# Optimization experiments

Hardware: AMD Instinct MI355X
Metric: run time of the kernel (lower is better)

The kernel has to match this reference:

```python
import jax, jax.numpy as jnp
import numpy as np
from jax import lax

# Geometry constants (stand-in for beijing* globals)
A = 96           # beijingAngleNum
P = 4            # beijingPlanes
DET0, DET1 = 256, 8   # beijingSubDetectorSize [u, v]
NZ, NY, NX = 32, 256, 256  # beijingVolumeSize (nz = P * DET1)
T = 256          # ray integration steps
LAMB = 0.01


def _bilinear(vol, ix, iy):
    # vol: [nz, ny, nx]; ix, iy: [...] index-space coords. Zero outside.
    nz, ny, nx = vol.shape
    x0 = jnp.floor(ix); y0 = jnp.floor(iy)
    fx = (ix - x0).astype(vol.dtype); fy = (iy - y0).astype(vol.dtype)
    x0i = x0.astype(jnp.int32); y0i = y0.astype(jnp.int32)

    def g(yi, xi):
        valid = ((xi >= 0) & (xi < nx) & (yi >= 0) & (yi < ny)).astype(vol.dtype)
        v = vol[:, jnp.clip(yi, 0, ny - 1), jnp.clip(xi, 0, nx - 1)]  # [nz, ...]
        return v * valid

    return (g(y0i, x0i) * (1 - fy) * (1 - fx)
            + g(y0i, x0i + 1) * (1 - fy) * fx
            + g(y0i + 1, x0i) * fy * (1 - fx)
            + g(y0i + 1, x0i + 1) * fy * fx)


def forward_project(vol):
    # vol: [NZ, NY, NX] -> sinogram [A, NZ, DET0], parallel-beam over 180 deg
    angles = jnp.arange(A, dtype=jnp.float32) * (np.pi / A)
    u = jnp.arange(DET0, dtype=jnp.float32) - (DET0 - 1) / 2.0  # detector coord
    t = jnp.arange(T, dtype=jnp.float32) - (T - 1) / 2.0        # along-ray coord

    def per_angle(_, th):
        c, s = jnp.cos(th), jnp.sin(th)
        x = -u[:, None] * s + t[None, :] * c   # [DET0, T]
        y = u[:, None] * c + t[None, :] * s
        samp = _bilinear(vol, x + (NX - 1) / 2.0, y + (NY - 1) / 2.0)  # [NZ,DET0,T]
        return None, samp.sum(-1)  # line integral, [NZ, DET0]

    _, S = lax.scan(per_angle, None, angles)
    return S  # [A, NZ, DET0]


def back_project(S):
    # S: [A, NZ, DET0] -> volume [NZ, NY, NX] (adjoint-style backprojection)
    angles = jnp.arange(A, dtype=jnp.float32) * (np.pi / A)
    yy = jnp.arange(NY, dtype=jnp.float32) - (NY - 1) / 2.0
    xx = jnp.arange(NX, dtype=jnp.float32) - (NX - 1) / 2.0
    Y, X = jnp.meshgrid(yy, xx, indexing='ij')  # [NY, NX]

    def per_angle(acc, inp):
        th, Sa = inp  # Sa: [NZ, DET0]
        c, s = jnp.cos(th), jnp.sin(th)
        ub = -X * s + Y * c + (DET0 - 1) / 2.0  # detector bin coord [NY,NX]
        u0 = jnp.floor(ub)
        fu = (ub - u0).astype(Sa.dtype)
        u0i = u0.astype(jnp.int32)

        def g(ui):
            valid = ((ui >= 0) & (ui < DET0)).astype(Sa.dtype)
            return Sa[:, jnp.clip(ui, 0, DET0 - 1)] * valid  # [NZ,NY,NX]

        val = g(u0i) * (1 - fu) + g(u0i + 1) * fu
        return acc + val, None

    vol0 = jnp.zeros((NZ, NY, NX), dtype=S.dtype)
    vol, _ = lax.scan(per_angle, vol0, (angles, S))
    return vol


def setup_inputs() -> dict:
    key = jax.random.key(0)
    k1, k2 = jax.random.split(key)
    x = jax.random.normal(k1, (1, 1, NZ, NY, NX), dtype=jnp.float32)
    p = jax.random.normal(k2, (1, 1, A * P, DET1, DET0), dtype=jnp.float32)
    return {"x": x, "p": p}


def reference(x, p):
    vol = x[0, 0]                              # [NZ, NY, NX]
    S = forward_project(vol)                   # [A, NZ, DET0] native
    # ForwardProjection wrapper: (A,P,V,U) -> permute -> flat external layout
    ext = S.reshape(A, P, DET1, DET0).transpose(0, 2, 1, 3).reshape(1, 1, A * P, DET1, DET0)
    residual = ext - p
    # BackProjection wrapper: undo external layout back to native
    res_native = residual.reshape(A, DET1, P, DET0).transpose(0, 2, 1, 3).reshape(A, NZ, DET0)
    volb = back_project(res_native)            # [NZ, NY, NX]
    return (-LAMB * volb)[None, None]          # [1,1,NZ,NY,NX]
```

## Files before the change

### kernel.cpp

```cpp
#include <hip/hip_runtime.h>
#include <hip/hip_fp16.h>

#define A     96
#define DET0  256
#define NZ    32
#define NY    256
#define NX    256
#define T     256
#define LAMB  0.01f

#define TRIG_OFF  0
#define REST_OFF  256
#define VOLB_OFF  786688
#define PART_OFF  1835264
#define RES_ELEMS 786432

__device__ __forceinline__ void accp_mix(float& a0, float& a1, unsigned v, float w) {
    asm("v_fma_mix_f32 %0, %2, %3, %0 op_sel:[0,0,0] op_sel_hi:[1,0,0]\n\t"
        "v_fma_mix_f32 %1, %2, %3, %1 op_sel:[1,0,0] op_sel_hi:[1,0,0]"
        : "+v"(a0), "+v"(a1)
        : "v"(v), "v"(w));
}
__device__ __forceinline__ void acc8h(float* acc, uint4 q, float w) {
    accp_mix(acc[0], acc[1], q.x, w);
    accp_mix(acc[2], acc[3], q.y, w);
    accp_mix(acc[4], acc[5], q.z, w);
    accp_mix(acc[6], acc[7], q.w, w);
}

__global__ __launch_bounds__(256) void k_transpose(const float* __restrict__ src,
                                                   unsigned short* __restrict__ vol_h,
                                                   float* __restrict__ trig,
                                                   const float* __restrict__ p,
                                                   float* __restrict__ res_t) {
    __shared__ float lds[64 * 33];
    const int y   = blockIdx.y;
    const int x0  = blockIdx.x * 64;
    const int tid = threadIdx.x;

    if (blockIdx.x == 0 && y == 0 && tid < A) {
        float th = (float)tid * (float)(3.14159265358979323846 / (double)A);
        trig[2 * tid]     = cosf(th);
        trig[2 * tid + 1] = sinf(th);
    }

    const int xr = tid & 63;
    const int zr = tid >> 6;
    #pragma unroll
    for (int pz = 0; pz < 8; ++pz) {
        int z = pz * 4 + zr;
        lds[xr * 33 + z] = src[(z * NY + y) * NX + x0 + xr];
    }
    __syncthreads();
    const int zw = tid & 31;
    const int xw = tid >> 5;
    #pragma unroll
    for (int px = 0; px < 8; ++px) {
        int xi = px * 8 + xw;
        vol_h[(y * NX + x0 + xi) * NZ + zw] =
            __half_as_ushort(__float2half(lds[xi * 33 + zw]));
    }

    if (y < A) {
        const int a  = y;
        const int u0 = blockIdx.x * 64;
        __syncthreads();
        const int col = tid & 63;
        const int r0  = tid >> 6;
        #pragma unroll
        for (int i = 0; i < 8; ++i) {
            int r = i * 4 + r0;
            lds[r * 65 + col] = p[a * 8192 + r * 256 + u0 + col];
        }
        __syncthreads();
        const int ul = tid >> 2;
        const int zb = (tid & 3) * 8;
        float o[8];
        #pragma unroll
        for (int k = 0; k < 8; ++k) {
            int z = zb + k;
            int r = ((z & 7) << 2) + (z >> 3);
            o[k] = -lds[r * 65 + ul];
        }
        float4* d = (float4*)(res_t + (a * DET0 + u0 + ul) * NZ + zb);
        d[0] = make_float4(o[0], o[1], o[2], o[3]);
        d[1] = make_float4(o[4], o[5], o[6], o[7]);
    }
}

__device__ __forceinline__ void rng(float g, float b, float L, float H,
                                    float& lo, float& hi) {
    if (fabsf(g) > 1e-5f) {
        float r0 = (L - b) / g, r1 = (H - b) / g;
        lo = fminf(r0, r1); hi = fmaxf(r0, r1);
    } else {
        bool in = (b >= L && b <= H);
        lo = in ? -1e9f : 1e9f;
        hi = in ? 1e9f : -1e9f;
    }
}
__device__ __forceinline__ int clampi(float v) {
    return (int)fminf(fmaxf(v, -2.f), 258.f);
}

__device__ __forceinline__ void sample_edge(const char* base, float ix, float iy,
                                            float* acc) {
    float xf = floorf(ix), yf = floorf(iy);
    float fx = ix - xf, fy = iy - yf;
    int x0 = (int)xf, y0 = (int)yf;
    float wx0 = 1.f - fx, wx1 = fx, wy0 = 1.f - fy, wy1 = fy;
    if ((unsigned)x0 >= NX)       wx0 = 0.f;
    if ((unsigned)(x0 + 1) >= NX) wx1 = 0.f;
    if ((unsigned)y0 >= NY)       wy0 = 0.f;
    if ((unsigned)(y0 + 1) >= NY) wy1 = 0.f;
    if ((wx0 == 0.f && wx1 == 0.f) || (wy0 == 0.f && wy1 == 0.f)) return;
    int cx0 = min(max(x0, 0), NX - 1);
    int cx1 = min(max(x0 + 1, 0), NX - 1);
    int cy0 = min(max(y0, 0), NY - 1);
    int cy1 = min(max(y0 + 1, 0), NY - 1);
    uint4 q00 = *(const uint4*)(base + ((size_t)((cy0 << 8) + cx0) << 6));
    uint4 q01 = *(const uint4*)(base + ((size_t)((cy0 << 8) + cx1) << 6));
    uint4 q10 = *(const uint4*)(base + ((size_t)((cy1 << 8) + cx0) << 6));
    uint4 q11 = *(const uint4*)(base + ((size_t)((cy1 << 8) + cx1) << 6));
    acc8h(acc, q00, wy0 * wx0);
    acc8h(acc, q01, wy0 * wx1);
    acc8h(acc, q10, wy1 * wx0);
    acc8h(acc, q11, wy1 * wx1);
}

__global__ __launch_bounds__(256) void k_forward(const unsigned short* __restrict__ vol_h,
                                                 const float* __restrict__ trig,
                                                 float* __restrict__ part) {
    const int tid = threadIdx.x;
    const int a   = blockIdx.z;
    const int u   = blockIdx.x * 64 + (tid >> 2);
    const int zq  = tid & 3;
    const int cid = blockIdx.y;
    const int C   = gridDim.y;

    const float c = trig[2 * a];
    const float s = trig[2 * a + 1];
    const float uu = (float)u - 127.5f;
    const float bx = fmaf(-uu, s, 127.5f);
    const float by = fmaf(uu, c, 127.5f);

    float lo1, hi1, lo2, hi2;
    rng(c, bx, -1.f, 256.f, lo1, hi1);
    rng(s, by, -1.f, 256.f, lo2, hi2);
    float fl = fmaxf(lo1, lo2), fh = fminf(hi1, hi2);
    int F0 = max(0,     clampi(ceilf(fl + 127.5f)));
    int F1 = min(T - 1, clampi(floorf(fh + 127.5f)));
    int len = F1 - F0 + 1; if (len < 0) len = 0;
    int b0 = F0 + (len * cid) / C;
    int b1 = F0 + (len * (cid + 1)) / C - 1;
    rng(c, bx, 1.f, 253.5f, lo1, hi1);
    rng(s, by, 1.f, 253.5f, lo2, hi2);
    float il = fmaxf(lo1, lo2), ih = fminf(hi1, hi2);
    int tI0 = max(clampi(ceilf(il + 127.5f)) + 1, b0);
    int tI1 = min(clampi(floorf(ih + 127.5f)) - 1, b1);
    if (tI0 > tI1) { tI0 = b1 + 1; tI1 = b1; }

    const char* base = (const char*)vol_h + zq * 16;
    float acc[8];
    #pragma unroll
    for (int k = 0; k < 8; ++k) acc[k] = 0.f;

    for (int t = b0; t < tI0; ++t) {
        float ttf = (float)t - 127.5f;
        sample_edge(base, fmaf(ttf, c, bx), fmaf(ttf, s, by), acc);
    }
    for (int t = tI0; t <= tI1; ++t) {
        float ttf = (float)t - 127.5f;
        float ix = fmaf(ttf, c, bx);
        float iy = fmaf(ttf, s, by);
        float xf = floorf(ix), yf = floorf(iy);
        float fx = ix - xf, fy = iy - yf;
        int row = ((int)yf << 8) + (int)xf;
        const char* p0 = base + ((size_t)row << 6);
        uint4 q00 = *(const uint4*)(p0);
        uint4 q01 = *(const uint4*)(p0 + 64);
        uint4 q10 = *(const uint4*)(p0 + 16384);
        uint4 q11 = *(const uint4*)(p0 + 16384 + 64);
        float wx0 = 1.f - fx, wy0 = 1.f - fy;
        acc8h(acc, q00, wy0 * wx0);
        acc8h(acc, q01, wy0 * fx);
        acc8h(acc, q10, fy * wx0);
        acc8h(acc, q11, fy * fx);
    }
    for (int t = tI1 + 1; t <= b1; ++t) {
        float ttf = (float)t - 127.5f;
        sample_edge(base, fmaf(ttf, c, bx), fmaf(ttf, s, by), acc);
    }

    float4* dst = (float4*)(part + (size_t)cid * RES_ELEMS +
                            ((a * DET0 + u) * NZ + zq * 8));
    dst[0] = make_float4(acc[0], acc[1], acc[2], acc[3]);
    dst[1] = make_float4(acc[4], acc[5], acc[6], acc[7]);
}

__global__ __launch_bounds__(256) void k_combine(const float* __restrict__ part,
                                                 float* __restrict__ res_t,
                                                 int C) {
    const int j4 = blockIdx.x * 256 + threadIdx.x;
    float4 v = ((const float4*)res_t)[j4];
    for (int c = 0; c < C; ++c) {
        float4 w = ((const float4*)(part + (size_t)c * RES_ELEMS))[j4];
        v.x += w.x; v.y += w.y; v.z += w.z; v.w += w.w;
    }
    ((float4*)res_t)[j4] = v;
}

__global__ __launch_bounds__(256) void k_backward(const float* __restrict__ res_t,
                                                  const float* __restrict__ trig,
                                                  float* __restrict__ out) {
    __shared__ float2 wbw[A * 32];
    __shared__ int    wbo[A * 32];
    __shared__ float  ob[32 * 33];
    const int tid = threadIdx.x;
    const int y  = blockIdx.y;
    const int xb = blockIdx.x * 32;

    for (int e = tid; e < A * 32; e += 256) {
        int a  = e >> 5;
        int xs = e & 31;
        float cc = trig[2 * a];
        float ss = trig[2 * a + 1];
        float xx = (float)(xb + xs) - 127.5f;
        float yy = (float)y - 127.5f;
        float ub = fmaf(-xx, ss, fmaf(yy, cc, 127.5f));
        float uf = floorf(ub);
        float fu = ub - uf;
        int i0 = (int)uf;
        float w0 = ((unsigned)i0 < DET0) ? (1.f - fu) : 0.f;
        float w1 = ((unsigned)(i0 + 1) < DET0) ? fu : 0.f;
        int c1 = min(max(i0 + 1, 0), DET0);
        wbw[e] = make_float2(w0, w1);
        wbo[e] = ((a * DET0 + c1) * NZ - NZ) << 2;
    }
    __syncthreads();

    const int xs = tid >> 3;
    const int zq = tid & 7;
    const char* rbase = (const char*)res_t + zq * 16;
    float4 acc = make_float4(0.f, 0.f, 0.f, 0.f);
    #pragma unroll 4
    for (int a = 0; a < A; ++a) {
        float2 w  = wbw[a * 32 + xs];
        int   off = wbo[a * 32 + xs];
        float4 v0 = *(const float4*)(rbase + off);
        float4 v1 = *(const float4*)(rbase + off + 128);
        acc.x = fmaf(w.x, v0.x, fmaf(w.y, v1.x, acc.x));
        acc.y = fmaf(w.x, v0.y, fmaf(w.y, v1.y, acc.y));
        acc.z = fmaf(w.x, v0.z, fmaf(w.y, v1.z, acc.z));
        acc.w = fmaf(w.x, v0.w, fmaf(w.y, v1.w, acc.w));
    }

    ob[(zq * 4 + 0) * 33 + xs] = acc.x;
    ob[(zq * 4 + 1) * 33 + xs] = acc.y;
    ob[(zq * 4 + 2) * 33 + xs] = acc.z;
    ob[(zq * 4 + 3) * 33 + xs] = acc.w;
    __syncthreads();

    const int z  = tid >> 3;
    const int x4 = (tid & 7) * 4;
    float4 o = make_float4(ob[z * 33 + x4],     ob[z * 33 + x4 + 1],
                           ob[z * 33 + x4 + 2], ob[z * 33 + x4 + 3]);
    float4* dst = (float4*)(out + (size_t)z * (NY * NX) + y * NX + xb + x4);
    *dst = make_float4(-LAMB * o.x, -LAMB * o.y, -LAMB * o.z, -LAMB * o.w);
}

extern "C" void kernel_launch(void* const* d_in, const int* in_sizes, int n_in,
                              void* d_out, int out_size, void* d_ws, size_t ws_size,
                              hipStream_t stream) {
    const float* x = (const float*)d_in[0];
    const float* p = (const float*)d_in[1];
    float* out = (float*)d_out;
    float* ws  = (float*)d_ws;

    float*          trig  = ws + TRIG_OFF;
    float*          res_t = ws + REST_OFF;
    unsigned short* vol_h = (unsigned short*)(ws + VOLB_OFF);
    float*          part  = ws + PART_OFF;

    size_t avail = ws_size / 4;
    int C = 8;
    while (C > 1 && (size_t)PART_OFF + (size_t)C * RES_ELEMS > avail) C >>= 1;

    k_transpose<<<dim3(NX / 64, NY), 256, 0, stream>>>(x, vol_h, trig, p, res_t);
    k_forward  <<<dim3(4, C, A), 256, 0, stream>>>(vol_h, trig, part);
    k_combine  <<<dim3(RES_ELEMS / 4 / 256), 256, 0, stream>>>(part, res_t, C);
    k_backward <<<dim3(NX / 32, NY), 256, 0, stream>>>(res_t, trig, out);
}
```

Measured before the change: 196.2 us.

## Stage per-angle detector windows in LDS with double buffering for backprojection

The backprojection kernel now handles two output rows per block. For each angle it computes the detector-bin window the 32x2 pixel tile touches and cooperatively loads that window of residual rows into XOR-swizzled shared memory, double-buffered so the next angle's global load overlaps the current angle's compute. This replaces the per-thread scattered global gathers and the precomputed weight tables with shared-memory reads and inline weight computation. The trade-offs are one barrier per angle, half as many blocks, and a fixed window size of 36 rows that has to cover every angle's footprint.

```diff
diff --git a/kernel.cpp b/kernel.cpp
--- a/kernel.cpp
+++ b/kernel.cpp
@@ -210,63 +210,135 @@
     ((float4*)res_t)[j4] = v;
 }
 
+#define BWIN 36
+#define BROW 144
 __global__ __launch_bounds__(256) void k_backward(const float* __restrict__ res_t,
                                                   const float* __restrict__ trig,
                                                   float* __restrict__ out) {
-    __shared__ float2 wbw[A * 32];
-    __shared__ int    wbo[A * 32];
-    __shared__ float  ob[32 * 33];
+    __shared__ float smem[2 * BWIN * (BROW / 4)];
     const int tid = threadIdx.x;
-    const int y  = blockIdx.y;
-    const int xb = blockIdx.x * 32;
-
-    for (int e = tid; e < A * 32; e += 256) {
-        int a  = e >> 5;
-        int xs = e & 31;
-        float cc = trig[2 * a];
-        float ss = trig[2 * a + 1];
-        float xx = (float)(xb + xs) - 127.5f;
-        float yy = (float)y - 127.5f;
-        float ub = fmaf(-xx, ss, fmaf(yy, cc, 127.5f));
-        float uf = floorf(ub);
-        float fu = ub - uf;
-        int i0 = (int)uf;
-        float w0 = ((unsigned)i0 < DET0) ? (1.f - fu) : 0.f;
-        float w1 = ((unsigned)(i0 + 1) < DET0) ? fu : 0.f;
-        int c1 = min(max(i0 + 1, 0), DET0);
-        wbw[e] = make_float2(w0, w1);
-        wbo[e] = ((a * DET0 + c1) * NZ - NZ) << 2;
-    }
+    const int xb  = blockIdx.x * 32;
+    const int y0  = blockIdx.y * 2;
+    const int xs  = tid >> 3;
+    const int zq  = tid & 7;
+    const float xt  = (float)(xb + xs) - 127.5f;
+    const float yt0 = (float)y0 - 127.5f;
+    const float yt1 = yt0 + 1.0f;
+    const float xlo = (float)xb - 127.5f;
+    const float xhi = (float)(xb + 31) - 127.5f;
+
+    float4 acc0 = make_float4(0.f, 0.f, 0.f, 0.f);
+    float4 acc1 = make_float4(0.f, 0.f, 0.f, 0.f);
+
+    #define WINDOW(aa, U0v, nchv) {                                        \
+        float cc_ = trig[2 * (aa)], ss_ = trig[2 * (aa) + 1];              \
+        float k0_ = fmaf(yt0, cc_, 127.5f);                                \
+        float k1_ = fmaf(yt1, cc_, 127.5f);                                \
+        float u00 = fmaf(-xlo, ss_, k0_), u01 = fmaf(-xhi, ss_, k0_);      \
+        float u10 = fmaf(-xlo, ss_, k1_), u11 = fmaf(-xhi, ss_, k1_);      \
+        float mn = fminf(fminf(u00, u01), fminf(u10, u11));                \
+        float mx = fmaxf(fmaxf(u00, u01), fmaxf(u10, u11));                \
+        U0v = (int)floorf(mn);                                             \
+        int rows_ = (int)floorf(mx) + 2 - U0v;   \
+        nchv = rows_ * 8;                         \
+    }
+    #define STAGE_LOAD(aa, U0v, nchv, r0, r1) {                            \
+        if (tid < (nchv)) {                                                \
+            int rr = tid >> 3, sl = tid & 7;                               \
+            int row = min(max((U0v) + rr, 0), DET0 - 1);                   \
+            r0 = *(const float4*)(res_t + (((aa) * DET0 + row) << 5) + sl * 4); \
+        }                                                                  \
+        if (tid + 256 < (nchv)) {                                          \
+            int cch = tid + 256;                                           \
+            int rr = cch >> 3, sl = cch & 7;                               \
+            int row = min(max((U0v) + rr, 0), DET0 - 1);                   \
+            r1 = *(const float4*)(res_t + (((aa) * DET0 + row) << 5) + sl * 4); \
+        }                                                                  \
+    }
+    #define STAGE_WRITE(bufv, nchv, r0, r1) {                              \
+        char* bb = (char*)(smem + (bufv) * (BWIN * BROW / 4));             \
+        if (tid < (nchv)) {                                                \
+            int rr = tid >> 3, sl = tid & 7;                               \
+            *(float4*)(bb + rr * BROW + ((sl ^ (rr & 7)) << 4)) = r0;      \
+        }                                                                  \
+        if (tid + 256 < (nchv)) {                                          \
+            int cch = tid + 256;                                           \
+            int rr = cch >> 3, sl = cch & 7;                               \
+            *(float4*)(bb + rr * BROW + ((sl ^ (rr & 7)) << 4)) = r1;      \
+        }                                                                  \
+    }
+
+    int U0c, nchc, U0n, nchn;
+    float4 s0, s1;
+    WINDOW(0, U0c, nchc);
+    STAGE_LOAD(0, U0c, nchc, s0, s1);
+    STAGE_WRITE(0, nchc, s0, s1);
     __syncthreads();
 
-    const int xs = tid >> 3;
-    const int zq = tid & 7;
-    const char* rbase = (const char*)res_t + zq * 16;
-    float4 acc = make_float4(0.f, 0.f, 0.f, 0.f);
-    #pragma unroll 4
     for (int a = 0; a < A; ++a) {
-        float2 w  = wbw[a * 32 + xs];
-        int   off = wbo[a * 32 + xs];
-        float4 v0 = *(const float4*)(rbase + off);
-        float4 v1 = *(const float4*)(rbase + off + 128);
-        acc.x = fmaf(w.x, v0.x, fmaf(w.y, v1.x, acc.x));
-        acc.y = fmaf(w.x, v0.y, fmaf(w.y, v1.y, acc.y));
-        acc.z = fmaf(w.x, v0.z, fmaf(w.y, v1.z, acc.z));
-        acc.w = fmaf(w.x, v0.w, fmaf(w.y, v1.w, acc.w));
-    }
-
-    ob[(zq * 4 + 0) * 33 + xs] = acc.x;
-    ob[(zq * 4 + 1) * 33 + xs] = acc.y;
-    ob[(zq * 4 + 2) * 33 + xs] = acc.z;
-    ob[(zq * 4 + 3) * 33 + xs] = acc.w;
-    __syncthreads();
-
-    const int z  = tid >> 3;
-    const int x4 = (tid & 7) * 4;
-    float4 o = make_float4(ob[z * 33 + x4],     ob[z * 33 + x4 + 1],
-                           ob[z * 33 + x4 + 2], ob[z * 33 + x4 + 3]);
-    float4* dst = (float4*)(out + (size_t)z * (NY * NX) + y * NX + xb + x4);
-    *dst = make_float4(-LAMB * o.x, -LAMB * o.y, -LAMB * o.z, -LAMB * o.w);
+        const int cur = a & 1;
+        if (a + 1 < A) {
+            WINDOW(a + 1, U0n, nchn);
+            STAGE_LOAD(a + 1, U0n, nchn, s0, s1);
+        }
+        const float cc = trig[2 * a];
+        const float ss = trig[2 * a + 1];
+        const char* bb = (const char*)(smem + cur * (BWIN * BROW / 4));
+        {
+            float ub = fmaf(-xt, ss, fmaf(yt0, cc, 127.5f));
+            float uf = floorf(ub);
+            float fu = ub - uf;
+            int i0 = (int)uf;
+            float w0 = ((unsigned)i0 < DET0) ? (1.f - fu) : 0.f;
+            float w1 = ((unsigned)(i0 + 1) < DET0) ? fu : 0.f;
+            int idx = i0 - U0c;
+            int id1 = idx + 1;
+            float4 v0 = *(const float4*)(bb + idx * BROW + ((zq ^ (idx & 7)) << 4));
+            float4 v1 = *(const float4*)(bb + id1 * BROW + ((zq ^ (id1 & 7)) << 4));
+            acc0.x = fmaf(w0, v0.x, fmaf(w1, v1.x, acc0.x));
+            acc0.y = fmaf(w0, v0.y, fmaf(w1, v1.y, acc0.y));
+            acc0.z = fmaf(w0, v0.z, fmaf(w1, v1.z, acc0.z));
+            acc0.w = fmaf(w0, v0.w, fmaf(w1, v1.w, acc0.w));
+        }
+        {
+            float ub = fmaf(-xt, ss, fmaf(yt1, cc, 127.5f));
+            float uf = floorf(ub);
+            float fu = ub - uf;
+            int i0 = (int)uf;
+            float w0 = ((unsigned)i0 < DET0) ? (1.f - fu) : 0.f;
+            float w1 = ((unsigned)(i0 + 1) < DET0) ? fu : 0.f;
+            int idx = i0 - U0c;
+            int id1 = idx + 1;
+            float4 v0 = *(const float4*)(bb + idx * BROW + ((zq ^ (idx & 7)) << 4));
+            float4 v1 = *(const float4*)(bb + id1 * BROW + ((zq ^ (id1 & 7)) << 4));
+            acc1.x = fmaf(w0, v0.x, fmaf(w1, v1.x, acc1.x));
+            acc1.y = fmaf(w0, v0.y, fmaf(w1, v1.y, acc1.y));
+            acc1.z = fmaf(w0, v0.z, fmaf(w1, v1.z, acc1.z));
+            acc1.w = fmaf(w0, v0.w, fmaf(w1, v1.w, acc1.w));
+        }
+        if (a + 1 < A) {
+            STAGE_WRITE(cur ^ 1, nchn, s0, s1);
+            U0c = U0n;
+        }
+        __syncthreads();
+    }
+
+    #pragma unroll 1
+    for (int yt = 0; yt < 2; ++yt) {
+        float4 acc = yt ? acc1 : acc0;
+        smem[(zq * 4 + 0) * 33 + xs] = acc.x;
+        smem[(zq * 4 + 1) * 33 + xs] = acc.y;
+        smem[(zq * 4 + 2) * 33 + xs] = acc.z;
+        smem[(zq * 4 + 3) * 33 + xs] = acc.w;
+        __syncthreads();
+        int z  = tid >> 3;
+        int x4 = (tid & 7) * 4;
+        float4 o = make_float4(smem[z * 33 + x4],     smem[z * 33 + x4 + 1],
+                               smem[z * 33 + x4 + 2], smem[z * 33 + x4 + 3]);
+        float4* dst = (float4*)(out + (size_t)z * (NY * NX) + (y0 + yt) * NX + xb + x4);
+        *dst = make_float4(-LAMB * o.x, -LAMB * o.y, -LAMB * o.z, -LAMB * o.w);
+        __syncthreads();
+    }
 }
 
 extern "C" void kernel_launch(void* const* d_in, const int* in_sizes, int n_in,
@@ -289,5 +361,5 @@
     k_transpose<<<dim3(NX / 64, NY), 256, 0, stream>>>(x, vol_h, trig, p, res_t);
     k_forward  <<<dim3(4, C, A), 256, 0, stream>>>(vol_h, trig, part);
     k_combine  <<<dim3(RES_ELEMS / 4 / 256), 256, 0, stream>>>(part, res_t, C);
-    k_backward <<<dim3(NX / 32, NY), 256, 0, stream>>>(res_t, trig, out);
-}
+    k_backward <<<dim3(NX / 32, NY / 2), 256, 0, stream>>>(res_t, trig, out);
+}
```

Measured after the change: 211.9 us. 1.08x slower.
